# Optimization experiments

Hardware: AMD Instinct MI355X
Metric: run time of the kernel (lower is better)

The kernel has to match this reference:

```python
import jax, jax.numpy as jnp
import numpy as np

B, S, D, H = 2, 2048, 1024, 16
DH = D // H


def setup_inputs() -> dict:
    key = jax.random.key(0)
    ks = jax.random.split(key, 5)
    scale = 0.02
    return {
        "X": jax.random.normal(ks[0], (B, S, D), jnp.float32),
        "Wq": jax.random.normal(ks[1], (H, D, DH), jnp.float32) * scale,
        "Wk": jax.random.normal(ks[2], (H, D, DH), jnp.float32) * scale,
        "Wv": jax.random.normal(ks[3], (H, D, DH), jnp.float32) * scale,
        "Wo": jax.random.normal(ks[4], (D, D), jnp.float32) * scale,
        "bo": jnp.zeros((D,), jnp.float32),
    }


def reference(X, Wq, Wk, Wv, Wo, bo):
    # Per-head projections, batched over heads: [B,H,S,DH]
    Q = jnp.einsum('bsd,hde->bhse', X, Wq)
    K = jnp.einsum('bsd,hde->bhse', X, Wk)
    V = jnp.einsum('bsd,hde->bhse', X, Wv)
    # Scores scaled by sqrt(d_model) exactly as in the source (not sqrt(d_head))
    A = jnp.einsum('bhse,bhte->bhst', Q, K) / jnp.sqrt(jnp.float32(D))
    A = jax.nn.softmax(A, axis=-1)  # no mask in the source
    O = jnp.einsum('bhst,bhte->bhse', A, V)  # [B,H,S,DH]
    # Concat heads -> [B,S,D], then output projection
    O = jnp.transpose(O, (0, 2, 1, 3)).reshape(B, S, D)
    return O @ Wo + bo
```

## Files before the change

kernel.cpp:

```cpp
#include <hip/hip_runtime.h>
#include <math.h>

static constexpr int Bc  = 2;
static constexpr int Sc  = 2048;
static constexpr int Dc  = 1024;
static constexpr int Hc  = 16;
static constexpr int DHc = 64;

typedef short bf16x8 __attribute__((ext_vector_type(8)));
typedef float f32x4  __attribute__((ext_vector_type(4)));

static constexpr float LOG2E = 1.4426950408889634f;

static __device__ __forceinline__ unsigned short f2bf(float x) {
  union { float f; unsigned u; } v; v.f = x;
  unsigned r = v.u + 0x7FFFu + ((v.u >> 16) & 1u);
  return (unsigned short)(r >> 16);
}
static __device__ __forceinline__ float bf2f(unsigned short u) {
  union { unsigned u; float f; } v; v.u = ((unsigned)u) << 16;
  return v.f;
}
static __device__ __forceinline__ unsigned pk2bf_trunc(float a, float b) {
  return __builtin_amdgcn_perm(__float_as_uint(b), __float_as_uint(a), 0x07060302u);
}
#if __has_builtin(__builtin_amdgcn_exp2f)
#define EXP2F(x) __builtin_amdgcn_exp2f(x)
#else
#define EXP2F(x) exp2f(x)
#endif

static __device__ __forceinline__ void gload16(const void* g, void* l) {
  __builtin_amdgcn_global_load_lds(
      (const __attribute__((address_space(1))) void*)g,
      (__attribute__((address_space(3))) void*)l, 16, 0, 0);
}

__global__ __launch_bounds__(256) void prep(
    const float* __restrict__ Wq, const float* __restrict__ Wk,
    const float* __restrict__ Wv, const float* __restrict__ Wo,
    const float* __restrict__ X,
    unsigned short* __restrict__ Wt3, unsigned short* __restrict__ Wot,
    unsigned short* __restrict__ Xb) {
  const int z = blockIdx.z;
  if (z == 4) {
    size_t base = ((size_t)blockIdx.y * 16 + blockIdx.x) * 4096;
#pragma unroll
    for (int it = 0; it < 16; ++it) {
      size_t i = base + it * 256 + threadIdx.x;
      float4 v = ((const float4*)X)[i];
      ushort4 u; u.x = f2bf(v.x); u.y = f2bf(v.y); u.z = f2bf(v.z); u.w = f2bf(v.w);
      ((ushort4*)Xb)[i] = u;
    }
    return;
  }
  __shared__ unsigned short T[64][68];
  const float* src; unsigned short* dst;
  int srcld, dstld, r0, c0;
  if (z < 3) {
    const float* W = (z == 0) ? Wq : (z == 1) ? Wk : Wv;
    unsigned short* Wt = Wt3 + (size_t)z * Dc * Dc;
    int h = blockIdx.y;
    src = W + (size_t)h * Dc * DHc;  srcld = DHc; r0 = blockIdx.x * 64; c0 = 0;
    dst = Wt + (size_t)h * DHc * Dc; dstld = Dc;
  } else {
    src = Wo;  srcld = Dc; r0 = blockIdx.x * 64; c0 = blockIdx.y * 64;
    dst = Wot; dstld = Dc;
  }
#pragma unroll
  for (int it = 0; it < 16; ++it) {
    int idx = it * 256 + threadIdx.x;
    int r = idx >> 6, c = idx & 63;
    T[c][r] = f2bf(src[(size_t)(r0 + r) * srcld + c0 + c]);
  }
  __syncthreads();
#pragma unroll
  for (int it = 0; it < 4; ++it) {
    int idx = it * 256 + threadIdx.x;
    int c = idx >> 4, r4 = (idx & 15) * 4;
    ushort4 u = *(const ushort4*)&T[c][r4];
    *(ushort4*)&dst[(size_t)(c0 + c) * dstld + r0 + r4] = u;
  }
}

__global__ __launch_bounds__(256) void qkv_gemm(
    const unsigned short* __restrict__ Xb, const unsigned short* __restrict__ Wt3,
    unsigned short* __restrict__ Qb, unsigned short* __restrict__ Kb,
    unsigned short* __restrict__ Vtb) {
  __shared__ alignas(16) unsigned char smem[35072];
  unsigned short (*As)[64] = (unsigned short(*)[64])smem;
  unsigned short (*Bs)[64] = (unsigned short(*)[64])(smem + 16384);

  const int tid = threadIdx.x;
  const int wv = tid >> 6, lane = tid & 63;
  const int ln = tid & 15, qd = (tid >> 4) & 3;
  const int wm = wv >> 1, wn = wv & 1;
  const int m0 = blockIdx.x * 128;
  const int y  = blockIdx.y;
  const int n0 = y * 128;
  const int which = y >> 3;
  const int lr = lane >> 3;
  const int lcs = ((lane & 7) ^ lr) * 8;

  f32x4 acc[4][4];
#pragma unroll
  for (int mt = 0; mt < 4; ++mt)
#pragma unroll
    for (int nt = 0; nt < 4; ++nt) acc[mt][nt] = (f32x4){0.f, 0.f, 0.f, 0.f};

  for (int k0 = 0; k0 < Dc; k0 += 64) {
    __syncthreads();
#pragma unroll
    for (int t = 0; t < 4; ++t) {
      gload16(Xb  + (size_t)(m0 + wv * 32 + t * 8 + lr) * Dc + k0 + lcs, &As[wv * 32 + t * 8][0]);
      gload16(Wt3 + (size_t)(n0 + wv * 32 + t * 8 + lr) * Dc + k0 + lcs, &Bs[wv * 32 + t * 8][0]);
    }
    __syncthreads();
#pragma unroll
    for (int ks = 0; ks < 2; ++ks) {
      const int pa = ((ks * 4 + qd) ^ (ln & 7)) * 8;
      bf16x8 af[4], bf[4];
#pragma unroll
      for (int mt = 0; mt < 4; ++mt)
        af[mt] = *(const bf16x8*)&As[wm * 64 + mt * 16 + ln][pa];
#pragma unroll
      for (int nt = 0; nt < 4; ++nt)
        bf[nt] = *(const bf16x8*)&Bs[wn * 64 + nt * 16 + ln][pa];
#pragma unroll
      for (int mt = 0; mt < 4; ++mt)
#pragma unroll
        for (int nt = 0; nt < 4; ++nt)
          acc[mt][nt] = __builtin_amdgcn_mfma_f32_16x16x32_bf16(af[mt], bf[nt], acc[mt][nt], 0, 0, 0);
    }
  }

  const int b = m0 >> 11, s0 = m0 & 2047;
  __syncthreads();

  if (which < 2) {
    unsigned short* Out = (which == 0) ? Qb : Kb;
    const float scale = (which == 0) ? (LOG2E / 32.0f) : 1.0f;
    unsigned short* Ts = (unsigned short*)smem;
#pragma unroll
    for (int mt = 0; mt < 4; ++mt)
#pragma unroll
      for (int r = 0; r < 4; ++r)
#pragma unroll
        for (int nt = 0; nt < 4; ++nt)
          Ts[(wm * 64 + mt * 16 + qd * 4 + r) * 136 + wn * 64 + nt * 16 + ln] =
              f2bf(acc[mt][nt][r] * scale);
    __syncthreads();
    const int row = tid >> 1;
    const int half = tid & 1;
    const int nbase = (n0 & 1023) + half * 64;
    const int h = nbase >> 6;
    unsigned short* gp = Out + (((size_t)b * Hc + h) * Sc + s0 + row) * DHc;
#pragma unroll
    for (int it = 0; it < 8; ++it) {
      ulonglong2 u = *(const ulonglong2*)&Ts[row * 136 + half * 64 + it * 8];
      *(ulonglong2*)&gp[it * 8] = u;
    }
  } else {
    unsigned short* Ts = (unsigned short*)smem;
    const int hb = (y & 7) * 2;
#pragma unroll
    for (int mt = 0; mt < 4; ++mt)
#pragma unroll
      for (int r = 0; r < 4; ++r)
#pragma unroll
        for (int nt = 0; nt < 4; ++nt)
          Ts[(wm * 64 + mt * 16 + qd * 4 + r) * 137 + wn * 64 + nt * 16 + ln] =
              f2bf(acc[mt][nt][r]);
    __syncthreads();
#pragma unroll
    for (int hh = 0; hh < 2; ++hh) {
      int bh = b * Hc + hb + hh;
#pragma unroll
      for (int it = 0; it < 8; ++it) {
        int idx = it * 256 + tid;
        int e = idx >> 5, s4 = (idx & 31) * 4;
        ushort4 u;
        u.x = Ts[(s4 + 0) * 137 + hh * 64 + e];
        u.y = Ts[(s4 + 1) * 137 + hh * 64 + e];
        u.z = Ts[(s4 + 2) * 137 + hh * 64 + e];
        u.w = Ts[(s4 + 3) * 137 + hh * 64 + e];
        *(ushort4*)&Vtb[((size_t)bh * DHc + e) * Sc + s0 + s4] = u;
      }
    }
  }
}

__global__ __launch_bounds__(256, 2) void attn_partial(
    const unsigned short* __restrict__ Qb, const unsigned short* __restrict__ Kb,
    const unsigned short* __restrict__ Vtb,
    unsigned short* __restrict__ Opart, float* __restrict__ lpart) {
  __shared__ alignas(16) unsigned short Ks[64][64];
  __shared__ alignas(16) unsigned short Vts[64][64];
  __shared__ alignas(16) unsigned short Ps[256][64];

  const int tid = threadIdx.x;
  const int wv = tid >> 6, lane = tid & 63;
  const int ln = tid & 15, qd = (tid >> 4) & 3;
  const int sT = blockIdx.x, bh = blockIdx.y, sp = blockIdx.z;
  const int lr = lane >> 3;
  const int lcs = ((lane & 7) ^ lr) * 8;

  bf16x8 qf[4][2];
  const size_t qrow0 = (size_t)bh * Sc + sT * 256 + wv * 64;
#pragma unroll
  for (int mt = 0; mt < 4; ++mt)
#pragma unroll
    for (int ks = 0; ks < 2; ++ks)
      qf[mt][ks] = *(const bf16x8*)&Qb[(qrow0 + mt * 16 + ln) * DHc + ks * 32 + qd * 8];

  bf16x8 vones;
#pragma unroll
  for (int j = 0; j < 8; ++j) vones[j] = (short)0x3F80;

  f32x4 o[4][4], lacc[4];
#pragma unroll
  for (int mt = 0; mt < 4; ++mt) {
    lacc[mt] = (f32x4){0.f, 0.f, 0.f, 0.f};
#pragma unroll
    for (int et = 0; et < 4; ++et) o[mt][et] = (f32x4){0.f, 0.f, 0.f, 0.f};
  }

  for (int kb = sp * 16; kb < sp * 16 + 16; ++kb) {
    __syncthreads();
#pragma unroll
    for (int t = 0; t < 2; ++t) {
      gload16(Kb  + ((size_t)bh * Sc + kb * 64 + wv * 16 + t * 8 + lr) * DHc + lcs,
              &Ks[wv * 16 + t * 8][0]);
      gload16(Vtb + ((size_t)bh * DHc + wv * 16 + t * 8 + lr) * Sc + kb * 64 + lcs,
              &Vts[wv * 16 + t * 8][0]);
    }
    __syncthreads();

    f32x4 st[4][4];
#pragma unroll
    for (int mt = 0; mt < 4; ++mt)
#pragma unroll
      for (int nt = 0; nt < 4; ++nt) st[mt][nt] = (f32x4){0.f, 0.f, 0.f, 0.f};
#pragma unroll
    for (int ks = 0; ks < 2; ++ks) {
      const int pa = ((ks * 4 + qd) ^ (ln & 7)) * 8;
#pragma unroll
      for (int nt = 0; nt < 4; ++nt) {
        bf16x8 kf = *(const bf16x8*)&Ks[nt * 16 + ln][pa];
#pragma unroll
        for (int mt = 0; mt < 4; ++mt)
          st[mt][nt] = __builtin_amdgcn_mfma_f32_16x16x32_bf16(kf, qf[mt][ks], st[mt][nt], 0, 0, 0);
      }
    }

#pragma unroll
    for (int mt = 0; mt < 4; ++mt) {
      const int prow = wv * 64 + mt * 16 + ln;
#pragma unroll
      for (int nt = 0; nt < 4; ++nt) {
        float p0 = EXP2F(st[mt][nt][0]);
        float p1 = EXP2F(st[mt][nt][1]);
        float p2 = EXP2F(st[mt][nt][2]);
        float p3 = EXP2F(st[mt][nt][3]);
        uint2 w;
        w.x = pk2bf_trunc(p0, p1);
        w.y = pk2bf_trunc(p2, p3);
        int ppos = ((2 * nt + (qd >> 1)) ^ (ln & 7)) * 8 + (qd & 1) * 4;
        *(uint2*)&Ps[prow][ppos] = w;
      }
    }
    __syncthreads();

#pragma unroll
    for (int ks = 0; ks < 2; ++ks) {
      const int pa = ((ks * 4 + qd) ^ (ln & 7)) * 8;
      bf16x8 pf[4];
#pragma unroll
      for (int mt = 0; mt < 4; ++mt) {
        pf[mt] = *(const bf16x8*)&Ps[wv * 64 + mt * 16 + ln][pa];
        lacc[mt] = __builtin_amdgcn_mfma_f32_16x16x32_bf16(pf[mt], vones, lacc[mt], 0, 0, 0);
      }
#pragma unroll
      for (int et = 0; et < 4; ++et) {
        bf16x8 vf = *(const bf16x8*)&Vts[et * 16 + ln][pa];
#pragma unroll
        for (int mt = 0; mt < 4; ++mt)
          o[mt][et] = __builtin_amdgcn_mfma_f32_16x16x32_bf16(pf[mt], vf, o[mt][et], 0, 0, 0);
      }
    }
  }

  const size_t pbase = (size_t)sp * 65536 + ((size_t)bh * 8 + sT) * 256;
  if (ln == 0) {
#pragma unroll
    for (int mt = 0; mt < 4; ++mt)
#pragma unroll
      for (int r = 0; r < 4; ++r)
        lpart[pbase + wv * 64 + mt * 16 + qd * 4 + r] = lacc[mt][r];
  }
#pragma unroll
  for (int mt = 0; mt < 4; ++mt)
#pragma unroll
    for (int r = 0; r < 4; ++r) {
      int row = wv * 64 + mt * 16 + qd * 4 + r;
#pragma unroll
      for (int et = 0; et < 4; ++et)
        Opart[(pbase + row) * DHc + et * 16 + ln] = f2bf(o[mt][et][r]);
    }
}

__global__ __launch_bounds__(256) void combine(
    const unsigned short* __restrict__ Opart, const float* __restrict__ lpart,
    unsigned short* __restrict__ Ocat) {
  const int sT = blockIdx.x, bh = blockIdx.y, tid = threadIdx.x;
  const int b = bh >> 4, h = bh & 15;
  const size_t p0 = ((size_t)bh * 8 + sT) * 256;
  const size_t p1 = p0 + 65536;
#pragma unroll
  for (int it = 0; it < 16; ++it) {
    int idx = it * 256 + tid;
    int row = idx >> 4, c4 = (idx & 15) * 4;
    ushort4 u0 = *(const ushort4*)&Opart[(p0 + row) * DHc + c4];
    ushort4 u1 = *(const ushort4*)&Opart[(p1 + row) * DHc + c4];
    float inv = 1.0f / (lpart[p0 + row] + lpart[p1 + row]);
    ushort4 w;
    w.x = f2bf((bf2f(u0.x) + bf2f(u1.x)) * inv);
    w.y = f2bf((bf2f(u0.y) + bf2f(u1.y)) * inv);
    w.z = f2bf((bf2f(u0.z) + bf2f(u1.z)) * inv);
    w.w = f2bf((bf2f(u0.w) + bf2f(u1.w)) * inv);
    *(ushort4*)&Ocat[((size_t)b * Sc + sT * 256 + row) * Dc + h * DHc + c4] = w;
  }
}

__global__ __launch_bounds__(256) void out_gemm(
    const unsigned short* __restrict__ Ab, const unsigned short* __restrict__ Wot,
    const float* __restrict__ bo, float* __restrict__ Out) {
  __shared__ alignas(16) unsigned short As[64][64];
  __shared__ alignas(16) unsigned short Bs[128][64];

  const int tid = threadIdx.x;
  const int wv = tid >> 6, lane = tid & 63;
  const int ln = tid & 15, qd = (tid >> 4) & 3;
  const int wm = wv >> 1, wn = wv & 1;
  const int m0 = blockIdx.x * 64, n0 = blockIdx.y * 128;
  const int lr = lane >> 3;
  const int lcs = ((lane & 7) ^ lr) * 8;

  f32x4 acc[2][4];
#pragma unroll
  for (int mt = 0; mt < 2; ++mt)
#pragma unroll
    for (int nt = 0; nt < 4; ++nt) acc[mt][nt] = (f32x4){0.f, 0.f, 0.f, 0.f};

  for (int k0 = 0; k0 < Dc; k0 += 64) {
    __syncthreads();
#pragma unroll
    for (int t = 0; t < 2; ++t)
      gload16(Ab + (size_t)(m0 + wv * 16 + t * 8 + lr) * Dc + k0 + lcs, &As[wv * 16 + t * 8][0]);
#pragma unroll
    for (int t = 0; t < 4; ++t)
      gload16(Wot + (size_t)(n0 + wv * 32 + t * 8 + lr) * Dc + k0 + lcs, &Bs[wv * 32 + t * 8][0]);
    __syncthreads();
#pragma unroll
    for (int ks = 0; ks < 2; ++ks) {
      const int pa = ((ks * 4 + qd) ^ (ln & 7)) * 8;
      bf16x8 af[2], bf[4];
#pragma unroll
      for (int mt = 0; mt < 2; ++mt)
        af[mt] = *(const bf16x8*)&As[wm * 32 + mt * 16 + ln][pa];
#pragma unroll
      for (int nt = 0; nt < 4; ++nt)
        bf[nt] = *(const bf16x8*)&Bs[wn * 64 + nt * 16 + ln][pa];
#pragma unroll
      for (int mt = 0; mt < 2; ++mt)
#pragma unroll
        for (int nt = 0; nt < 4; ++nt)
          acc[mt][nt] = __builtin_amdgcn_mfma_f32_16x16x32_bf16(af[mt], bf[nt], acc[mt][nt], 0, 0, 0);
    }
  }

  float bias[4];
#pragma unroll
  for (int nt = 0; nt < 4; ++nt) bias[nt] = bo[n0 + wn * 64 + nt * 16 + ln];

#pragma unroll
  for (int mt = 0; mt < 2; ++mt)
#pragma unroll
    for (int r = 0; r < 4; ++r) {
      int m = m0 + wm * 32 + mt * 16 + qd * 4 + r;
#pragma unroll
      for (int nt = 0; nt < 4; ++nt)
        Out[(size_t)m * Dc + n0 + wn * 64 + nt * 16 + ln] = acc[mt][nt][r] + bias[nt];
    }
}

extern "C" void kernel_launch(void* const* d_in, const int* in_sizes, int n_in,
                              void* d_out, int out_size, void* d_ws, size_t ws_size,
                              hipStream_t stream) {
  (void)in_sizes; (void)n_in; (void)out_size; (void)ws_size;
  const float* X  = (const float*)d_in[0];
  const float* Wq = (const float*)d_in[1];
  const float* Wk = (const float*)d_in[2];
  const float* Wv = (const float*)d_in[3];
  const float* Wo = (const float*)d_in[4];
  const float* bo = (const float*)d_in[5];
  float* out = (float*)d_out;

  const size_t nX = (size_t)Bc * Sc * Dc;
  unsigned short* Xb    = (unsigned short*)d_ws;
  unsigned short* Wt3   = Xb + nX;
  unsigned short* Wot   = Wt3 + (size_t)3 * Dc * Dc;
  unsigned short* Qb    = Wot + (size_t)Dc * Dc;
  unsigned short* Kb    = Qb + nX;
  unsigned short* Vtb   = Kb + nX;
  unsigned short* Opart = Vtb + nX;
  float* lpart = (float*)(Opart + 2 * nX);
  unsigned short* Ocat = Xb;

  prep<<<dim3(16, 16, 5), 256, 0, stream>>>(Wq, Wk, Wv, Wo, X, Wt3, Wot, Xb);
  qkv_gemm<<<dim3(32, 24), 256, 0, stream>>>(Xb, Wt3, Qb, Kb, Vtb);
  attn_partial<<<dim3(8, 32, 2), 256, 0, stream>>>(Qb, Kb, Vtb, Opart, lpart);
  combine<<<dim3(8, 32), 256, 0, stream>>>(Opart, lpart, Ocat);
  out_gemm<<<dim3(64, 8), 256, 0, stream>>>(Ocat, Wot, bo, out);
}
```

Baseline: 190.3 us.

## Rewrite QKV GEMM as 256x256 tile with 8 waves and pipelined LDS staging

```diff
diff --git a/kernel.cpp b/kernel.cpp
--- a/kernel.cpp
+++ b/kernel.cpp
@@ -83,111 +83,178 @@
   }
 }
 
-__global__ __launch_bounds__(256) void qkv_gemm(
+__global__ __launch_bounds__(512, 2) void qkv_gemm(
     const unsigned short* __restrict__ Xb, const unsigned short* __restrict__ Wt3,
     unsigned short* __restrict__ Qb, unsigned short* __restrict__ Kb,
     unsigned short* __restrict__ Vtb) {
-  __shared__ alignas(16) unsigned char smem[35072];
-  unsigned short (*As)[64] = (unsigned short(*)[64])smem;
-  unsigned short (*Bs)[64] = (unsigned short(*)[64])(smem + 16384);
+  __shared__ alignas(16) unsigned char smem[135168];
+  unsigned short (*S)[64] = (unsigned short(*)[64])smem;
 
   const int tid = threadIdx.x;
   const int wv = tid >> 6, lane = tid & 63;
-  const int ln = tid & 15, qd = (tid >> 4) & 3;
-  const int wm = wv >> 1, wn = wv & 1;
-  const int m0 = blockIdx.x * 128;
-  const int y  = blockIdx.y;
-  const int n0 = y * 128;
-  const int which = y >> 3;
+  const int ln = lane & 15, qd = (lane >> 4) & 3;
+  const int wm = wv >> 2, wn = wv & 3;
   const int lr = lane >> 3;
-  const int lcs = ((lane & 7) ^ lr) * 8;
-
-  f32x4 acc[4][4];
-#pragma unroll
-  for (int mt = 0; mt < 4; ++mt)
+  const int gcol = ((lane & 7) ^ lr) * 8;
+  const int paq = ln & 7;
+
+  const int bid = blockIdx.x;
+  const int l = (bid & 7) * 24 + (bid >> 3);
+  const int xb = l & 15, y = l >> 4;
+  const int m0 = xb * 256, n0 = y * 256;
+  const int which = y >> 2;
+  const int b = m0 >> 11, s0 = m0 & 2047;
+  const int h0 = (y & 3) * 4;
+
+  const unsigned short* Ap = Xb + (size_t)m0 * 1024;
+  const unsigned short* Bp = Wt3 + (size_t)n0 * 1024;
+  const int grow = wv * 16 + lr;
+
+#define STG(gb, srow) do {                                                  \
+    gload16((gb) + (size_t)grow * 1024 + gcol,       &S[(srow) + wv * 16][0]); \
+    gload16((gb) + (size_t)(grow + 8) * 1024 + gcol, &S[(srow) + wv * 16 + 8][0]); \
+  } while (0)
+
+#define RD_A(mh, rowbase) do {                                              \
+    _Pragma("unroll") for (int mt = 0; mt < 4; ++mt)                        \
+      _Pragma("unroll") for (int ks = 0; ks < 2; ++ks)                      \
+        af[mt][ks] = *(const bf16x8*)&S[(rowbase) + (mh) * 64 + mt * 16 + ln] \
+                                       [((ks * 4 + qd) ^ paq) * 8];         \
+  } while (0)
+
+#define RD_B(nh, rowbase) do {                                              \
+    _Pragma("unroll") for (int nt = 0; nt < 2; ++nt)                        \
+      _Pragma("unroll") for (int ks = 0; ks < 2; ++ks)                      \
+        bf[(nh) * 2 + nt][ks] = *(const bf16x8*)&S[(rowbase) + (nh) * 32 + nt * 16 + ln] \
+                                                  [((ks * 4 + qd) ^ paq) * 8]; \
+  } while (0)
+
+#define MM(mh, nh) do {                                                     \
+    _Pragma("unroll") for (int ks = 0; ks < 2; ++ks)                        \
+      _Pragma("unroll") for (int mt = 0; mt < 4; ++mt)                      \
+        _Pragma("unroll") for (int nt = 0; nt < 2; ++nt)                    \
+          acc[(mh) * 4 + mt][(nh) * 2 + nt] =                               \
+              __builtin_amdgcn_mfma_f32_16x16x32_bf16(                      \
+                  af[mt][ks], bf[(nh) * 2 + nt][ks],                        \
+                  acc[(mh) * 4 + mt][(nh) * 2 + nt], 0, 0, 0);              \
+  } while (0)
+
+#define BAR __builtin_amdgcn_s_barrier()
+#define WAITL asm volatile("s_waitcnt lgkmcnt(0)" ::: "memory")
+#define WAITV(n) asm volatile("s_waitcnt vmcnt(" #n ")" ::: "memory")
+#define PRIO1 __builtin_amdgcn_s_setprio(1)
+#define PRIO0 __builtin_amdgcn_s_setprio(0)
+
+  f32x4 acc[8][4];
+#pragma unroll
+  for (int mt = 0; mt < 8; ++mt)
 #pragma unroll
     for (int nt = 0; nt < 4; ++nt) acc[mt][nt] = (f32x4){0.f, 0.f, 0.f, 0.f};
 
-  for (int k0 = 0; k0 < Dc; k0 += 64) {
-    __syncthreads();
-#pragma unroll
-    for (int t = 0; t < 4; ++t) {
-      gload16(Xb  + (size_t)(m0 + wv * 32 + t * 8 + lr) * Dc + k0 + lcs, &As[wv * 32 + t * 8][0]);
-      gload16(Wt3 + (size_t)(n0 + wv * 32 + t * 8 + lr) * Dc + k0 + lcs, &Bs[wv * 32 + t * 8][0]);
-    }
-    __syncthreads();
-#pragma unroll
-    for (int ks = 0; ks < 2; ++ks) {
-      const int pa = ((ks * 4 + qd) ^ (ln & 7)) * 8;
-      bf16x8 af[4], bf[4];
-#pragma unroll
-      for (int mt = 0; mt < 4; ++mt)
-        af[mt] = *(const bf16x8*)&As[wm * 64 + mt * 16 + ln][pa];
-#pragma unroll
-      for (int nt = 0; nt < 4; ++nt)
-        bf[nt] = *(const bf16x8*)&Bs[wn * 64 + nt * 16 + ln][pa];
-#pragma unroll
-      for (int mt = 0; mt < 4; ++mt)
-#pragma unroll
-        for (int nt = 0; nt < 4; ++nt)
-          acc[mt][nt] = __builtin_amdgcn_mfma_f32_16x16x32_bf16(af[mt], bf[nt], acc[mt][nt], 0, 0, 0);
-    }
-  }
-
-  const int b = m0 >> 11, s0 = m0 & 2047;
-  __syncthreads();
-
+  STG(Bp, 512);
+  STG(Ap, 0);
+  STG(Ap + 128 * 1024, 128);
+  STG(Bp + 128 * 1024, 640);
+  STG(Bp + 64, 768);
+  STG(Ap + 64, 256);
+  WAITV(4);
+  BAR;
+
+  bf16x8 af[4][2], bf[4][2];
+
+  for (int j = 0; j < 8; ++j) {
+    const int last = (j == 7);
+    const unsigned short* Ak = Ap + j * 128;
+    const unsigned short* Bk = Bp + j * 128;
+
+    STG(Ak + 128 * 1024 + 64, 384);
+    RD_A(0, wm * 128);
+    RD_B(0, 512 + (wn >> 1) * 128 + (wn & 1) * 64);
+    BAR; WAITL;
+    PRIO1; MM(0, 0); PRIO0; BAR;
+    STG(Bk + 128 * 1024 + 64, 896);
+    RD_B(1, 512 + (wn >> 1) * 128 + (wn & 1) * 64);
+    BAR; WAITL;
+    PRIO1; MM(0, 1); PRIO0; BAR;
+    if (!last) STG(Bk + 128, 512);
+    RD_A(1, wm * 128);
+    BAR; WAITL;
+    PRIO1; MM(1, 0); PRIO0; BAR;
+    if (!last) STG(Ak + 128, 0);
+    BAR;
+    PRIO1; MM(1, 1); PRIO0;
+    if (last) { WAITV(0); } else { WAITV(4); }
+    BAR;
+
+    if (!last) STG(Ak + 128 * 1024 + 128, 128);
+    RD_A(0, 256 + wm * 128);
+    RD_B(0, 768 + (wn >> 1) * 128 + (wn & 1) * 64);
+    BAR; WAITL;
+    PRIO1; MM(0, 0); PRIO0; BAR;
+    if (!last) STG(Bk + 128 * 1024 + 128, 640);
+    RD_B(1, 768 + (wn >> 1) * 128 + (wn & 1) * 64);
+    BAR; WAITL;
+    PRIO1; MM(0, 1); PRIO0; BAR;
+    if (!last) STG(Bk + 192, 768);
+    RD_A(1, 256 + wm * 128);
+    BAR; WAITL;
+    PRIO1; MM(1, 0); PRIO0; BAR;
+    if (!last) STG(Ak + 192, 256);
+    BAR;
+    PRIO1; MM(1, 1); PRIO0;
+    if (!last) WAITV(4);
+    BAR;
+  }
+
+  unsigned short* Ts = (unsigned short*)smem;
   if (which < 2) {
     unsigned short* Out = (which == 0) ? Qb : Kb;
     const float scale = (which == 0) ? (LOG2E / 32.0f) : 1.0f;
-    unsigned short* Ts = (unsigned short*)smem;
-#pragma unroll
-    for (int mt = 0; mt < 4; ++mt)
-#pragma unroll
-      for (int r = 0; r < 4; ++r)
-#pragma unroll
-        for (int nt = 0; nt < 4; ++nt)
-          Ts[(wm * 64 + mt * 16 + qd * 4 + r) * 136 + wn * 64 + nt * 16 + ln] =
+#pragma unroll
+    for (int mt = 0; mt < 8; ++mt)
+#pragma unroll
+      for (int nt = 0; nt < 4; ++nt)
+#pragma unroll
+        for (int r = 0; r < 4; ++r)
+          Ts[(wm * 128 + mt * 16 + qd * 4 + r) * 264 + wn * 64 + nt * 16 + ln] =
               f2bf(acc[mt][nt][r] * scale);
     __syncthreads();
     const int row = tid >> 1;
-    const int half = tid & 1;
-    const int nbase = (n0 & 1023) + half * 64;
-    const int h = nbase >> 6;
-    unsigned short* gp = Out + (((size_t)b * Hc + h) * Sc + s0 + row) * DHc;
-#pragma unroll
-    for (int it = 0; it < 8; ++it) {
-      ulonglong2 u = *(const ulonglong2*)&Ts[row * 136 + half * 64 + it * 8];
-      *(ulonglong2*)&gp[it * 8] = u;
+#pragma unroll
+    for (int it = 0; it < 16; ++it) {
+      int c16 = (tid & 1) * 16 + it;
+      int head = c16 >> 3, e8 = c16 & 7;
+      *(ulonglong2*)&Out[(((size_t)b * Hc + h0 + head) * Sc + s0 + row) * DHc + e8 * 8] =
+          *(const ulonglong2*)&Ts[row * 264 + c16 * 8];
     }
   } else {
-    unsigned short* Ts = (unsigned short*)smem;
-    const int hb = (y & 7) * 2;
-#pragma unroll
-    for (int mt = 0; mt < 4; ++mt)
-#pragma unroll
-      for (int r = 0; r < 4; ++r)
-#pragma unroll
-        for (int nt = 0; nt < 4; ++nt)
-          Ts[(wm * 64 + mt * 16 + qd * 4 + r) * 137 + wn * 64 + nt * 16 + ln] =
+#pragma unroll
+    for (int mt = 0; mt < 8; ++mt)
+#pragma unroll
+      for (int nt = 0; nt < 4; ++nt)
+#pragma unroll
+        for (int r = 0; r < 4; ++r)
+          Ts[(wn * 64 + nt * 16 + ln) * 264 + wm * 128 + mt * 16 + qd * 4 + r] =
               f2bf(acc[mt][nt][r]);
     __syncthreads();
-#pragma unroll
-    for (int hh = 0; hh < 2; ++hh) {
-      int bh = b * Hc + hb + hh;
-#pragma unroll
-      for (int it = 0; it < 8; ++it) {
-        int idx = it * 256 + tid;
-        int e = idx >> 5, s4 = (idx & 31) * 4;
-        ushort4 u;
-        u.x = Ts[(s4 + 0) * 137 + hh * 64 + e];
-        u.y = Ts[(s4 + 1) * 137 + hh * 64 + e];
-        u.z = Ts[(s4 + 2) * 137 + hh * 64 + e];
-        u.w = Ts[(s4 + 3) * 137 + hh * 64 + e];
-        *(ushort4*)&Vtb[((size_t)bh * DHc + e) * Sc + s0 + s4] = u;
-      }
-    }
-  }
+    const int n = tid >> 1;
+    const int head = n >> 6, e = n & 63;
+    unsigned short* dst = Vtb + (((size_t)b * Hc + h0 + head) * DHc + e) * Sc + s0;
+#pragma unroll
+    for (int it = 0; it < 16; ++it) {
+      int s16 = (tid & 1) * 16 + it;
+      *(ulonglong2*)&dst[s16 * 8] = *(const ulonglong2*)&Ts[n * 264 + s16 * 8];
+    }
+  }
+#undef STG
+#undef RD_A
+#undef RD_B
+#undef MM
+#undef BAR
+#undef WAITL
+#undef WAITV
+#undef PRIO1
+#undef PRIO0
 }
 
 __global__ __launch_bounds__(256, 2) void attn_partial(
@@ -418,7 +485,7 @@
   unsigned short* Ocat = Xb;
 
   prep<<<dim3(16, 16, 5), 256, 0, stream>>>(Wq, Wk, Wv, Wo, X, Wt3, Wot, Xb);
-  qkv_gemm<<<dim3(32, 24), 256, 0, stream>>>(Xb, Wt3, Qb, Kb, Vtb);
+  qkv_gemm<<<dim3(192), 512, 0, stream>>>(Xb, Wt3, Qb, Kb, Vtb);
   attn_partial<<<dim3(8, 32, 2), 256, 0, stream>>>(Qb, Kb, Vtb, Opart, lpart);
   combine<<<dim3(8, 32), 256, 0, stream>>>(Opart, lpart, Ocat);
   out_gemm<<<dim3(64, 8), 256, 0, stream>>>(Ocat, Wot, bo, out);
```

Result: faster. 183.9 us (-3.4%).
